# Performance work log

Measured on AMD Instinct MI355X. Metric: run time of the kernel, lower is better.

Reference implementation:

```python
import jax, jax.numpy as jnp
import numpy as np

OUT_F, IN_F = 11008, 4096
B, S = 2, 2048


def setup_inputs() -> dict:
    key = jax.random.key(0)
    k1, k2, k3 = jax.random.split(key, 3)
    x = jax.random.normal(k1, (B, S, IN_F), dtype=jnp.float32)
    # int8-valued quantized weight stored in int32 carrier, range [-128, 127]
    weight_q = jax.random.randint(k2, (OUT_F, IN_F), 0, 255, dtype=jnp.int32) - 128
    # realistic per-tensor quant params: small positive scale, zero_point near 0
    scale = jnp.float32(0.01)
    zero_point = jnp.float32(3.0)
    return {"x": x, "weight_q": weight_q, "scale": scale, "zero_point": zero_point}


def reference(x, weight_q, scale, zero_point):
    # Dequantize: w = scale * (q - zero_point)  -> [out_f, in_f] float32
    w = scale * (weight_q.astype(jnp.float32) - zero_point)
    # F.linear(x, w) = x @ w.T  -> [B, S, out_f]
    return jnp.einsum('bsi,oi->bso', x, w)
```

## Files before the change

### kernel.cpp

```cpp
#include <hip/hip_runtime.h>


#define M_DIM 4096
#define N_DIM 11008
#define K_DIM 4096
#define KT8 32
#define NT_N 43
#define NT_M 16

typedef __attribute__((ext_vector_type(4))) int i32x4;
typedef __attribute__((ext_vector_type(4))) float f32x4;

__device__ inline unsigned short f2bf(float f) {
  unsigned int u = __float_as_uint(f);
  u += 0x7FFFu + ((u >> 16) & 1u);
  return (unsigned short)(u >> 16);
}

__global__ __launch_bounds__(256) void cvt_w_i8(const int* __restrict__ q,
                                                int4* __restrict__ wb, int n16) {
  int stride = gridDim.x * blockDim.x;
  for (int i = blockIdx.x * blockDim.x + threadIdx.x; i < n16; i += stride) {
    const int4* s = (const int4*)q + (size_t)i * 4;
    int4 a = s[0], b = s[1], c = s[2], d = s[3];
    int4 o;
    o.x = (a.x & 0xff) | ((a.y & 0xff) << 8) | ((a.z & 0xff) << 16) | ((a.w & 0xff) << 24);
    o.y = (b.x & 0xff) | ((b.y & 0xff) << 8) | ((b.z & 0xff) << 16) | ((b.w & 0xff) << 24);
    o.z = (c.x & 0xff) | ((c.y & 0xff) << 8) | ((c.z & 0xff) << 16) | ((c.w & 0xff) << 24);
    o.w = (d.x & 0xff) | ((d.y & 0xff) << 8) | ((d.z & 0xff) << 16) | ((d.w & 0xff) << 24);
    wb[i] = o;
  }
}

__global__ __launch_bounds__(256) void cvt_x_i8(const float* __restrict__ x,
                                                int4* __restrict__ xb,
                                                float* __restrict__ sx,
                                                float* __restrict__ rs) {
  const int row = blockIdx.x;
  const float* xr = x + (size_t)row * K_DIM;
  const int t = threadIdx.x;
  float4 v[4];
  float amax = 0.f, sum = 0.f;
#pragma unroll
  for (int j = 0; j < 4; ++j) {
    v[j] = *(const float4*)(xr + t * 16 + j * 4);
    amax = fmaxf(amax, fmaxf(fmaxf(fabsf(v[j].x), fabsf(v[j].y)),
                             fmaxf(fabsf(v[j].z), fabsf(v[j].w))));
    sum += (v[j].x + v[j].y) + (v[j].z + v[j].w);
  }
#pragma unroll
  for (int off = 1; off < 64; off <<= 1) {
    amax = fmaxf(amax, __shfl_xor(amax, off, 64));
    sum += __shfl_xor(sum, off, 64);
  }
  __shared__ float smx[4], sms[4];
  const int wv = t >> 6, ln = t & 63;
  if (ln == 0) { smx[wv] = amax; sms[wv] = sum; }
  __syncthreads();
  const float gmax = fmaxf(fmaxf(smx[0], smx[1]), fmaxf(smx[2], smx[3]));
  const float gsum = (sms[0] + sms[1]) + (sms[2] + sms[3]);
  const float gm = fmaxf(gmax, 1e-30f);
  const float qs = 127.f / gm;
  int b[16];
#pragma unroll
  for (int j = 0; j < 4; ++j) {
    b[j * 4 + 0] = (int)rintf(v[j].x * qs);
    b[j * 4 + 1] = (int)rintf(v[j].y * qs);
    b[j * 4 + 2] = (int)rintf(v[j].z * qs);
    b[j * 4 + 3] = (int)rintf(v[j].w * qs);
  }
  int4 o;
  o.x = (b[0] & 0xff) | ((b[1] & 0xff) << 8) | ((b[2] & 0xff) << 16) | ((b[3] & 0xff) << 24);
  o.y = (b[4] & 0xff) | ((b[5] & 0xff) << 8) | ((b[6] & 0xff) << 16) | ((b[7] & 0xff) << 24);
  o.z = (b[8] & 0xff) | ((b[9] & 0xff) << 8) | ((b[10] & 0xff) << 16) | ((b[11] & 0xff) << 24);
  o.w = (b[12] & 0xff) | ((b[13] & 0xff) << 8) | ((b[14] & 0xff) << 16) | ((b[15] & 0xff) << 24);
  xb[((size_t)row * K_DIM >> 4) + t] = o;
  if (t == 0) { sx[row] = gm / 127.f; rs[row] = gsum; }
}


__device__ __forceinline__ void stage_half(const char* __restrict__ gsrc,
                                           char* ldsBase, int w, int lane) {
  const int rsub = lane >> 3;
  const int csw  = ((lane & 7) ^ rsub) << 4;
#pragma unroll
  for (int r = 0; r < 2; ++r) {
    __builtin_amdgcn_global_load_lds(
        (const __attribute__((address_space(1))) void*)(
            gsrc + (size_t)(r * 64 + w * 8 + rsub) * K_DIM + csw),
        (__attribute__((address_space(3))) void*)(ldsBase + r * 8192 + w * 1024),
        16, 0, 0);
  }
}

#define DS_A(d, mh)                                                                 \
  do {                                                                              \
    _Pragma("unroll") for (int mi = 0; mi < 4; ++mi) {                              \
      _Pragma("unroll") for (int kk = 0; kk < 2; ++kk) {                            \
        a_frag[mi][kk] = *(const i32x4*)(ldsB + (d) * 65536 + aHalf + aRow +        \
                                         ((mh) * 4 + mi) * 2048 + kc[kk]);          \
      }                                                                             \
    }                                                                               \
  } while (0)

#define DS_B2(d, nh)                                                                \
  do {                                                                              \
    _Pragma("unroll") for (int ni = 0; ni < 2; ++ni) {                              \
      _Pragma("unroll") for (int kk = 0; kk < 2; ++kk) {                            \
        b_frag[(nh) * 2 + ni][kk] =                                                 \
            *(const i32x4*)(ldsB + (d) * 65536 + bHalf + bRow +                     \
                            ((nh) * 2 + ni) * 2048 + kc[kk]);                       \
      }                                                                             \
    }                                                                               \
  } while (0)

#define MFMA_QUAD(mh, nh)                                                           \
  do {                                                                              \
    _Pragma("unroll") for (int mi = 0; mi < 4; ++mi) {                              \
      _Pragma("unroll") for (int ni = 0; ni < 2; ++ni) {                            \
        _Pragma("unroll") for (int kk = 0; kk < 2; ++kk) {                          \
          acc[(mh) * 4 + mi][(nh) * 2 + ni] =                                       \
              __builtin_amdgcn_mfma_i32_16x16x64_i8(                                \
                  a_frag[mi][kk], b_frag[(nh) * 2 + ni][kk],                        \
                  acc[(mh) * 4 + mi][(nh) * 2 + ni], 0, 0, 0);                      \
        }                                                                           \
      }                                                                             \
    }                                                                               \
  } while (0)

#define PHASE_BAR() asm volatile("s_barrier" ::: "memory")
#define VMC4() asm volatile("s_waitcnt vmcnt(4)")

__global__ __launch_bounds__(512, 2) void qgemm_i8(const char* __restrict__ Ai8,
                                                   const char* __restrict__ Wi8,
                                                   const float* __restrict__ sx,
                                                   const float* __restrict__ rs,
                                                   const float* __restrict__ sp,
                                                   const float* __restrict__ zpp,
                                                   float* __restrict__ C) {
  __shared__ char lds[131072];

  int bid = blockIdx.x;
  {
    const int cpx = (NT_M * NT_N) >> 3;
    bid = (bid & 7) * cpx + (bid >> 3);
  }
  const int mt = bid / NT_N;
  const int nt = bid % NT_N;

  const int tid  = threadIdx.x;
  const int w    = tid >> 6;
  const int lane = tid & 63;
  const int l15  = lane & 15;
  const int l4   = lane >> 4;
  const int wr   = w >> 2;
  const int wc   = w & 3;

  const char* gA = Ai8 + (size_t)(mt * 256) * K_DIM;
  const char* gB = Wi8 + (size_t)(nt * 256) * K_DIM;

  const char* ldsB = (const char*)lds;
  const unsigned aHalf = (unsigned)wr * 16384u;
  const unsigned bHalf = 32768u + (unsigned)(wc >> 1) * 16384u;
  const unsigned aRow  = (unsigned)l15 * 128u;
  const unsigned bRow  = (unsigned)((wc & 1) * 64 + l15) * 128u;
  const unsigned swz   = (unsigned)(l15 & 7) << 4;
  const unsigned kc[2] = {((unsigned)(l4 * 16)) ^ swz,
                          ((unsigned)(64 + l4 * 16)) ^ swz};

  i32x4 a_frag[4][2];
  i32x4 b_frag[4][2];
  i32x4 acc[8][4];
#pragma unroll
  for (int m = 0; m < 8; ++m)
#pragma unroll
    for (int n = 0; n < 4; ++n) acc[m][n] = (i32x4)0;

  stage_half(gB, lds + 32768, w, lane);
  stage_half(gB + (size_t)128 * K_DIM, lds + 49152, w, lane);
  stage_half(gA, lds + 0, w, lane);
  stage_half(gA + (size_t)128 * K_DIM, lds + 16384, w, lane);
  stage_half(gB + 128, lds + 98304, w, lane);
  stage_half(gB + (size_t)128 * K_DIM + 128, lds + 114688, w, lane);
  VMC4();
  PHASE_BAR();

#pragma unroll 1
  for (int i = 0; i < KT8 / 2; ++i) {
    const int t1 = 2 * i + 1;
    const int c2 = (2 * i + 2 < KT8) ? 2 * i + 2 : KT8 - 1;
    const int c3 = (2 * i + 3 < KT8) ? 2 * i + 3 : KT8 - 1;

    DS_A(0, 0);
    DS_B2(0, 0);
    DS_B2(0, 1);
    PHASE_BAR();
    stage_half(gA + (size_t)t1 * 128, lds + 65536, w, lane);
    stage_half(gA + (size_t)128 * K_DIM + (size_t)t1 * 128, lds + 81920, w, lane);
    __builtin_amdgcn_s_setprio(1);
    MFMA_QUAD(0, 0);
    MFMA_QUAD(0, 1);
    __builtin_amdgcn_s_setprio(0);

    DS_A(0, 1);
    PHASE_BAR();
    stage_half(gB + (size_t)c2 * 128, lds + 32768, w, lane);
    stage_half(gB + (size_t)128 * K_DIM + (size_t)c2 * 128, lds + 49152, w, lane);
    __builtin_amdgcn_s_setprio(1);
    MFMA_QUAD(1, 1);
    MFMA_QUAD(1, 0);
    __builtin_amdgcn_s_setprio(0);
    VMC4();
    PHASE_BAR();

    DS_A(1, 0);
    DS_B2(1, 0);
    DS_B2(1, 1);
    PHASE_BAR();
    stage_half(gA + (size_t)c2 * 128, lds + 0, w, lane);
    stage_half(gA + (size_t)128 * K_DIM + (size_t)c2 * 128, lds + 16384, w, lane);
    __builtin_amdgcn_s_setprio(1);
    MFMA_QUAD(0, 0);
    MFMA_QUAD(0, 1);
    __builtin_amdgcn_s_setprio(0);

    DS_A(1, 1);
    PHASE_BAR();
    stage_half(gB + (size_t)c3 * 128, lds + 98304, w, lane);
    stage_half(gB + (size_t)128 * K_DIM + (size_t)c3 * 128, lds + 114688, w, lane);
    __builtin_amdgcn_s_setprio(1);
    MFMA_QUAD(1, 1);
    MFMA_QUAD(1, 0);
    __builtin_amdgcn_s_setprio(0);
    VMC4();
    PHASE_BAR();
  }

  const float s   = *sp;
  const float szp = s * (*zpp);
  const int grow = mt * 256 + wr * 128 + l4 * 4;
  const int gcol = nt * 256 + wc * 64 + l15;
#pragma unroll
  for (int ma = 0; ma < 8; ++ma) {
#pragma unroll
    for (int j = 0; j < 4; ++j) {
      const int m = grow + ma * 16 + j;
      const float alpha = s * sx[m];
      const float beta  = szp * rs[m];
#pragma unroll
      for (int n = 0; n < 4; ++n)
        C[(size_t)m * N_DIM + (gcol + n * 16)] =
            fmaf(alpha, (float)acc[ma][n][j], -beta);
    }
  }
}


typedef __attribute__((ext_vector_type(8))) short short8_t;

__global__ __launch_bounds__(256) void qgemm_fused(const float* __restrict__ Ap,
                                                   const int* __restrict__ Bp,
                                                   const float* __restrict__ sp,
                                                   const float* __restrict__ zpp,
                                                   float* __restrict__ C) {
  __shared__ unsigned short As[128 * 64];
  __shared__ unsigned short Bs[128 * 64];
  int bid = blockIdx.x;
  {
    const int nwg = gridDim.x;
    if ((nwg & 7) == 0) bid = (bid & 7) * (nwg >> 3) + (bid >> 3);
  }
  const int mt = bid / (N_DIM / 128);
  const int nt = bid % (N_DIM / 128);
  const int tid = threadIdx.x, wave = tid >> 6, lane = tid & 63;
  const int l15 = lane & 15, l4 = lane >> 4, wr = wave >> 1, wcc = wave & 1;
  f32x4 acc[4][4];
#pragma unroll
  for (int m = 0; m < 4; ++m)
#pragma unroll
    for (int n = 0; n < 4; ++n) acc[m][n] = (f32x4)0.0f;
  const unsigned swz = (unsigned)(lane & 7) << 4;
  const unsigned aBase = (unsigned)(wr * 64 + l15) * 128;
  const unsigned bBase = (unsigned)(wcc * 64 + l15) * 128;
  const unsigned kc0 = ((unsigned)(l4 * 16)) ^ swz;
  const unsigned kc1 = ((unsigned)(64 + l4 * 16)) ^ swz;
  const char* AsB = (const char*)As;
  const char* BsB = (const char*)Bs;
  const float sc = *sp;
  const float nszp = -sc * (*zpp);
  for (int t = 0; t < K_DIM / 64; ++t) {
#pragma unroll
    for (int i = 0; i < 8; ++i) {
      const int c = i * 256 + tid;
      const int row = c >> 4, col = (c & 15) * 4;
      float4 v = *(const float4*)(Ap + (size_t)(mt * 128 + row) * K_DIM + t * 64 + col);
      ushort4 o = make_ushort4(f2bf(v.x), f2bf(v.y), f2bf(v.z), f2bf(v.w));
      const unsigned off = (unsigned)row * 128 +
                           (((unsigned)col * 2) ^ (((unsigned)(row & 7)) << 4));
      *(ushort4*)((char*)As + off) = o;
    }
#pragma unroll
    for (int i = 0; i < 8; ++i) {
      const int c = i * 256 + tid;
      const int row = c >> 4, col = (c & 15) * 4;
      int4 v = *(const int4*)(Bp + (size_t)(nt * 128 + row) * K_DIM + t * 64 + col);
      ushort4 o = make_ushort4(f2bf(fmaf(sc, (float)v.x, nszp)),
                               f2bf(fmaf(sc, (float)v.y, nszp)),
                               f2bf(fmaf(sc, (float)v.z, nszp)),
                               f2bf(fmaf(sc, (float)v.w, nszp)));
      const unsigned off = (unsigned)row * 128 +
                           (((unsigned)col * 2) ^ (((unsigned)(row & 7)) << 4));
      *(ushort4*)((char*)Bs + off) = o;
    }
    __syncthreads();
#pragma unroll
    for (int kk = 0; kk < 2; ++kk) {
      const unsigned kcx = kk ? kc1 : kc0;
      short8_t af[4], bfr[4];
#pragma unroll
      for (int m = 0; m < 4; ++m) af[m] = *(const short8_t*)(AsB + aBase + m * 2048 + kcx);
#pragma unroll
      for (int n = 0; n < 4; ++n) bfr[n] = *(const short8_t*)(BsB + bBase + n * 2048 + kcx);
#pragma unroll
      for (int m = 0; m < 4; ++m)
#pragma unroll
        for (int n = 0; n < 4; ++n)
          acc[m][n] = __builtin_amdgcn_mfma_f32_16x16x32_bf16(af[m], bfr[n], acc[m][n], 0, 0, 0);
    }
    __syncthreads();
  }
  const int grow = mt * 128 + wr * 64 + l4 * 4;
  const int gcol = nt * 128 + wcc * 64 + l15;
#pragma unroll
  for (int m = 0; m < 4; ++m)
#pragma unroll
    for (int n = 0; n < 4; ++n)
#pragma unroll
      for (int j = 0; j < 4; ++j)
        C[(size_t)(grow + m * 16 + j) * N_DIM + (gcol + n * 16)] = acc[m][n][j];
}

extern "C" void kernel_launch(void* const* d_in, const int* in_sizes, int n_in,
                              void* d_out, int out_size, void* d_ws, size_t ws_size,
                              hipStream_t stream) {
  const float* x   = (const float*)d_in[0];
  const int*   wq  = (const int*)d_in[1];
  const float* sp  = (const float*)d_in[2];
  const float* zpp = (const float*)d_in[3];
  float* out = (float*)d_out;

  const size_t wbytes = (size_t)N_DIM * K_DIM;
  const size_t xbytes = (size_t)M_DIM * K_DIM;
  const size_t need   = wbytes + xbytes + 2 * (size_t)M_DIM * sizeof(float);

  if (ws_size >= need) {
    char*  wb = (char*)d_ws;
    char*  xb = (char*)d_ws + wbytes;
    float* sx = (float*)((char*)d_ws + wbytes + xbytes);
    float* rs = sx + M_DIM;
    cvt_w_i8<<<2048, 256, 0, stream>>>(wq, (int4*)wb,
                                       (int)((size_t)N_DIM * K_DIM / 16));
    cvt_x_i8<<<M_DIM, 256, 0, stream>>>(x, (int4*)xb, sx, rs);
    qgemm_i8<<<NT_M * NT_N, 512, 0, stream>>>(xb, wb, sx, rs, sp, zpp, out);
  } else {
    qgemm_fused<<<(M_DIM / 128) * (N_DIM / 128), 256, 0, stream>>>(x, wq, sp, zpp, out);
  }
}
```

Measured before the change: 256.2 us.

## Shrink int8 GEMM tile to 256x128 with K=64 steps and 4 waves

Changes the block tile from 256x256 with 8 waves and 128-byte K slices to 256x128 with 4 waves and 64-byte K slices. LDS drops from 128KB to 48KB, and the staging layout and swizzle are rewritten to match. The grid doubles to 1376 blocks, which gives better occupancy and wave balance. The cost is less data reuse per block, so more global traffic, and twice as many barrier-separated steps.

```diff
diff --git a/kernel.cpp b/kernel.cpp
--- a/kernel.cpp
+++ b/kernel.cpp
@@ -4,8 +4,8 @@
 #define M_DIM 4096
 #define N_DIM 11008
 #define K_DIM 4096
-#define KT8 32
-#define NT_N 43
+#define KT64 64
+#define NT_N 86
 #define NT_M 16
 
 typedef __attribute__((ext_vector_type(4))) int i32x4;
@@ -81,14 +81,14 @@
 
 __device__ __forceinline__ void stage_half(const char* __restrict__ gsrc,
                                            char* ldsBase, int w, int lane) {
-  const int rsub = lane >> 3;
-  const int csw  = ((lane & 7) ^ rsub) << 4;
-#pragma unroll
-  for (int r = 0; r < 2; ++r) {
+  const int sl = ((lane & 3) ^ ((lane >> 3) & 3)) << 4;
+#pragma unroll
+  for (int p = 0; p < 2; ++p) {
+    const int r = p * 64 + w * 16 + (lane >> 2);
     __builtin_amdgcn_global_load_lds(
         (const __attribute__((address_space(1))) void*)(
-            gsrc + (size_t)(r * 64 + w * 8 + rsub) * K_DIM + csw),
-        (__attribute__((address_space(3))) void*)(ldsBase + r * 8192 + w * 1024),
+            gsrc + (size_t)r * K_DIM + sl),
+        (__attribute__((address_space(3))) void*)(ldsBase + p * 4096 + w * 1024),
         16, 0, 0);
   }
 }
@@ -96,21 +96,16 @@
 #define DS_A(d, mh)                                                                 \
   do {                                                                              \
     _Pragma("unroll") for (int mi = 0; mi < 4; ++mi) {                              \
-      _Pragma("unroll") for (int kk = 0; kk < 2; ++kk) {                            \
-        a_frag[mi][kk] = *(const i32x4*)(ldsB + (d) * 65536 + aHalf + aRow +        \
-                                         ((mh) * 4 + mi) * 2048 + kc[kk]);          \
-      }                                                                             \
+      a_frag[mi] = *(const i32x4*)(ldsB + (d) * 24576 + aBase +                     \
+                                   ((mh) * 4 + mi) * 1024);                         \
     }                                                                               \
   } while (0)
 
-#define DS_B2(d, nh)                                                                \
+#define DS_B4(d)                                                                    \
   do {                                                                              \
-    _Pragma("unroll") for (int ni = 0; ni < 2; ++ni) {                              \
-      _Pragma("unroll") for (int kk = 0; kk < 2; ++kk) {                            \
-        b_frag[(nh) * 2 + ni][kk] =                                                 \
-            *(const i32x4*)(ldsB + (d) * 65536 + bHalf + bRow +                     \
-                            ((nh) * 2 + ni) * 2048 + kc[kk]);                       \
-      }                                                                             \
+    _Pragma("unroll") for (int ni = 0; ni < 4; ++ni) {                              \
+      b_frag[ni] = *(const i32x4*)(ldsB + (d) * 24576 + 16384 + bBase +             \
+                                   ni * 1024);                                      \
     }                                                                               \
   } while (0)
 
@@ -118,27 +113,25 @@
   do {                                                                              \
     _Pragma("unroll") for (int mi = 0; mi < 4; ++mi) {                              \
       _Pragma("unroll") for (int ni = 0; ni < 2; ++ni) {                            \
-        _Pragma("unroll") for (int kk = 0; kk < 2; ++kk) {                          \
-          acc[(mh) * 4 + mi][(nh) * 2 + ni] =                                       \
-              __builtin_amdgcn_mfma_i32_16x16x64_i8(                                \
-                  a_frag[mi][kk], b_frag[(nh) * 2 + ni][kk],                        \
-                  acc[(mh) * 4 + mi][(nh) * 2 + ni], 0, 0, 0);                      \
-        }                                                                           \
+        acc[(mh) * 4 + mi][(nh) * 2 + ni] =                                         \
+            __builtin_amdgcn_mfma_i32_16x16x64_i8(                                  \
+                a_frag[mi], b_frag[(nh) * 2 + ni],                                  \
+                acc[(mh) * 4 + mi][(nh) * 2 + ni], 0, 0, 0);                        \
       }                                                                             \
     }                                                                               \
   } while (0)
 
 #define PHASE_BAR() asm volatile("s_barrier" ::: "memory")
-#define VMC4() asm volatile("s_waitcnt vmcnt(4)")
-
-__global__ __launch_bounds__(512, 2) void qgemm_i8(const char* __restrict__ Ai8,
+#define VMC2() asm volatile("s_waitcnt vmcnt(2)")
+
+__global__ __launch_bounds__(256, 2) void qgemm_i8(const char* __restrict__ Ai8,
                                                    const char* __restrict__ Wi8,
                                                    const float* __restrict__ sx,
                                                    const float* __restrict__ rs,
                                                    const float* __restrict__ sp,
                                                    const float* __restrict__ zpp,
                                                    float* __restrict__ C) {
-  __shared__ char lds[131072];
+  __shared__ char lds[49152];
 
   int bid = blockIdx.x;
   {
@@ -153,50 +146,44 @@
   const int lane = tid & 63;
   const int l15  = lane & 15;
   const int l4   = lane >> 4;
-  const int wr   = w >> 2;
-  const int wc   = w & 3;
+  const int wr   = w >> 1;
+  const int wc   = w & 1;
 
   const char* gA = Ai8 + (size_t)(mt * 256) * K_DIM;
-  const char* gB = Wi8 + (size_t)(nt * 256) * K_DIM;
-
+  const char* gB = Wi8 + (size_t)(nt * 128) * K_DIM;
+  char* ldsc = lds;
   const char* ldsB = (const char*)lds;
-  const unsigned aHalf = (unsigned)wr * 16384u;
-  const unsigned bHalf = 32768u + (unsigned)(wc >> 1) * 16384u;
-  const unsigned aRow  = (unsigned)l15 * 128u;
-  const unsigned bRow  = (unsigned)((wc & 1) * 64 + l15) * 128u;
-  const unsigned swz   = (unsigned)(l15 & 7) << 4;
-  const unsigned kc[2] = {((unsigned)(l4 * 16)) ^ swz,
-                          ((unsigned)(64 + l4 * 16)) ^ swz};
-
-  i32x4 a_frag[4][2];
-  i32x4 b_frag[4][2];
+
+  const unsigned swz16 = (unsigned)((l4 ^ ((l15 >> 1) & 3)) << 4);
+  const unsigned aBase = (unsigned)wr * 8192u + (unsigned)l15 * 64u + swz16;
+  const unsigned bBase = (unsigned)wc * 4096u + (unsigned)l15 * 64u + swz16;
+
+  i32x4 a_frag[4];
+  i32x4 b_frag[4];
   i32x4 acc[8][4];
 #pragma unroll
   for (int m = 0; m < 8; ++m)
 #pragma unroll
     for (int n = 0; n < 4; ++n) acc[m][n] = (i32x4)0;
 
-  stage_half(gB, lds + 32768, w, lane);
-  stage_half(gB + (size_t)128 * K_DIM, lds + 49152, w, lane);
-  stage_half(gA, lds + 0, w, lane);
-  stage_half(gA + (size_t)128 * K_DIM, lds + 16384, w, lane);
-  stage_half(gB + 128, lds + 98304, w, lane);
-  stage_half(gB + (size_t)128 * K_DIM + 128, lds + 114688, w, lane);
-  VMC4();
+  stage_half(gB, ldsc + 16384, w, lane);
+  stage_half(gA, ldsc + 0, w, lane);
+  stage_half(gA + (size_t)128 * K_DIM, ldsc + 8192, w, lane);
+  stage_half(gB + 64, ldsc + 24576 + 16384, w, lane);
+  VMC2();
   PHASE_BAR();
 
 #pragma unroll 1
-  for (int i = 0; i < KT8 / 2; ++i) {
+  for (int i = 0; i < KT64 / 2; ++i) {
     const int t1 = 2 * i + 1;
-    const int c2 = (2 * i + 2 < KT8) ? 2 * i + 2 : KT8 - 1;
-    const int c3 = (2 * i + 3 < KT8) ? 2 * i + 3 : KT8 - 1;
+    const int c2 = (2 * i + 2 < KT64) ? 2 * i + 2 : KT64 - 1;
+    const int c3 = (2 * i + 3 < KT64) ? 2 * i + 3 : KT64 - 1;
 
     DS_A(0, 0);
-    DS_B2(0, 0);
-    DS_B2(0, 1);
-    PHASE_BAR();
-    stage_half(gA + (size_t)t1 * 128, lds + 65536, w, lane);
-    stage_half(gA + (size_t)128 * K_DIM + (size_t)t1 * 128, lds + 81920, w, lane);
+    DS_B4(0);
+    PHASE_BAR();
+    stage_half(gA + (size_t)t1 * 64, ldsc + 24576, w, lane);
+    stage_half(gA + (size_t)128 * K_DIM + (size_t)t1 * 64, ldsc + 24576 + 8192, w, lane);
     __builtin_amdgcn_s_setprio(1);
     MFMA_QUAD(0, 0);
     MFMA_QUAD(0, 1);
@@ -204,21 +191,19 @@
 
     DS_A(0, 1);
     PHASE_BAR();
-    stage_half(gB + (size_t)c2 * 128, lds + 32768, w, lane);
-    stage_half(gB + (size_t)128 * K_DIM + (size_t)c2 * 128, lds + 49152, w, lane);
+    stage_half(gB + (size_t)c2 * 64, ldsc + 16384, w, lane);
     __builtin_amdgcn_s_setprio(1);
     MFMA_QUAD(1, 1);
     MFMA_QUAD(1, 0);
     __builtin_amdgcn_s_setprio(0);
-    VMC4();
+    VMC2();
     PHASE_BAR();
 
     DS_A(1, 0);
-    DS_B2(1, 0);
-    DS_B2(1, 1);
-    PHASE_BAR();
-    stage_half(gA + (size_t)c2 * 128, lds + 0, w, lane);
-    stage_half(gA + (size_t)128 * K_DIM + (size_t)c2 * 128, lds + 16384, w, lane);
+    DS_B4(1);
+    PHASE_BAR();
+    stage_half(gA + (size_t)c2 * 64, ldsc + 0, w, lane);
+    stage_half(gA + (size_t)128 * K_DIM + (size_t)c2 * 64, ldsc + 8192, w, lane);
     __builtin_amdgcn_s_setprio(1);
     MFMA_QUAD(0, 0);
     MFMA_QUAD(0, 1);
@@ -226,20 +211,19 @@
 
     DS_A(1, 1);
     PHASE_BAR();
-    stage_half(gB + (size_t)c3 * 128, lds + 98304, w, lane);
-    stage_half(gB + (size_t)128 * K_DIM + (size_t)c3 * 128, lds + 114688, w, lane);
+    stage_half(gB + (size_t)c3 * 64, ldsc + 24576 + 16384, w, lane);
     __builtin_amdgcn_s_setprio(1);
     MFMA_QUAD(1, 1);
     MFMA_QUAD(1, 0);
     __builtin_amdgcn_s_setprio(0);
-    VMC4();
+    VMC2();
     PHASE_BAR();
   }
 
   const float s   = *sp;
   const float szp = s * (*zpp);
   const int grow = mt * 256 + wr * 128 + l4 * 4;
-  const int gcol = nt * 256 + wc * 64 + l15;
+  const int gcol = nt * 128 + wc * 64 + l15;
 #pragma unroll
   for (int ma = 0; ma < 8; ++ma) {
 #pragma unroll
@@ -361,7 +345,7 @@
     cvt_w_i8<<<2048, 256, 0, stream>>>(wq, (int4*)wb,
                                        (int)((size_t)N_DIM * K_DIM / 16));
     cvt_x_i8<<<M_DIM, 256, 0, stream>>>(x, (int4*)xb, sx, rs);
-    qgemm_i8<<<NT_M * NT_N, 512, 0, stream>>>(xb, wb, sx, rs, sp, zpp, out);
+    qgemm_i8<<<NT_M * NT_N, 256, 0, stream>>>(xb, wb, sx, rs, sp, zpp, out);
   } else {
     qgemm_fused<<<(M_DIM / 128) * (N_DIM / 128), 256, 0, stream>>>(x, wq, sp, zpp, out);
   }
```

After: 271.5 us. 1.06x slower.
